# Kernel tuning notes

Measured on AMD Instinct MI355X. Metric: run time of the kernel, lower is better.

Reference implementation:

```python
import jax, jax.numpy as jnp
import numpy as np
from jax import lax

B, N, S, K = 16, 8192, 1024, 32
FACTOR = 1.0
EPS_BN = 1e-5


def farthest_point_sample(xyz, npoint):
    # xyz: [B, N, 3] -> idx [B, npoint]. Deterministic start at index 0
    # (torch version starts at a random index; start choice doesn't change the math pattern).
    b, n, _ = xyz.shape
    bidx = jnp.arange(b)

    def step(carry, _):
        distance, farthest = carry
        centroid = xyz[bidx, farthest]                      # [B, 3]
        dist = jnp.sum((xyz - centroid[:, None, :]) ** 2, -1)  # [B, N]
        distance = jnp.minimum(distance, dist)
        new_far = jnp.argmax(distance, axis=-1)
        return (distance, new_far), farthest

    init = (jnp.full((b, n), 1e10, xyz.dtype), jnp.zeros((b,), jnp.int32))
    _, idxs = lax.scan(step, init, None, length=npoint)
    return idxs.T  # [B, npoint]


def square_distance(src, dst):
    # [B,Ns,3] x [B,Nd,3] -> [B,Ns,Nd]
    d = -2.0 * jnp.einsum('bnc,bmc->bnm', src, dst)
    d += jnp.sum(src ** 2, -1)[:, :, None]
    d += jnp.sum(dst ** 2, -1)[:, None, :]
    return d


def safe_cdist(x):
    # x: [B, C, S]; pairwise euclidean over rows -> [B, C, C]; zero-safe sqrt
    diff = x[:, :, None, :] - x[:, None, :, :]          # [B, C, C, S]
    sq = jnp.sum(diff * diff, -1)
    pos = sq > 0
    return jnp.where(pos, jnp.sqrt(jnp.where(pos, sq, 1.0)), 0.0)


def batchnorm(x, gamma, beta, axes):
    mean = jnp.mean(x, axes, keepdims=True)
    var = jnp.var(x, axes, keepdims=True)  # biased, as in torch BN normalization
    return (x - mean) / jnp.sqrt(var + EPS_BN) * gamma + beta


def reference(xyz, bn1_gamma, bn1_beta, bn2_gamma, bn2_beta):
    b = xyz.shape[0]
    # --- FPS sampling ---
    fps_idx = farthest_point_sample(lax.stop_gradient(xyz), S)          # [B,S]
    new_xyz = jnp.take_along_axis(xyz, fps_idx[:, :, None], axis=1)     # [B,S,3]
    # --- kNN grouping ---
    sq = square_distance(lax.stop_gradient(new_xyz), lax.stop_gradient(xyz))  # [B,S,N]
    _, knn_idx = lax.top_k(-sq, K)                                      # [B,S,K] indices
    grouped = jax.vmap(lambda p, i: p[i])(xyz, knn_idx)                 # [B,S,K,3]
    diff = grouped - new_xyz[:, :, None, :]
    std = jnp.std(diff, ddof=1)                                         # scalar, unbiased like torch.std
    knn_norm = diff / (std + 1e-5)
    center = jnp.broadcast_to(new_xyz[:, :, None, :], (b, S, K, 3))
    knn_xyz = jnp.concatenate([knn_norm, center], axis=-1)              # [B,S,K,6]
    # --- Pooling over neighbors ---
    x = jnp.transpose(knn_xyz, (0, 3, 1, 2))                            # [B,6,S,K]
    lc = jnp.max(x, -1) + jnp.mean(x, -1)                               # [B,6,S]
    lc = jax.nn.relu(batchnorm(lc, bn1_gamma[None, :, None], bn1_beta[None, :, None], (0, 2)))
    # --- Consecutive representation (cdist + superdiagonal factor) ---
    tfcw = safe_cdist(lc)                                               # [B,6,6]
    i = jnp.arange(5)
    tfcw = tfcw.at[:, i, i + 1].multiply(FACTOR)
    # --- Pooling2 ---
    feat = tfcw.reshape(b, -1)                                          # [B,36]
    feat = jax.nn.relu(batchnorm(feat, bn2_gamma[None, :], bn2_beta[None, :], (0,)))
    return feat


def setup_inputs() -> dict:
    key = jax.random.key(0)
    k1, = jax.random.split(key, 1)
    return {
        'xyz': jax.random.normal(k1, (B, N, 3), dtype=jnp.float32),
        'bn1_gamma': jnp.ones((6,), jnp.float32),
        'bn1_beta': jnp.zeros((6,), jnp.float32),
        'bn2_gamma': jnp.ones((36,), jnp.float32),
        'bn2_beta': jnp.zeros((36,), jnp.float32),
    }
```

## Files before the change

kernel.cpp:

```cpp
#include <hip/hip_runtime.h>
#include <hip/hip_bf16.h>

constexpr int BB = 16;
constexpr int NN = 8192;
constexpr int SS = 1024;
constexpr int KK = 32;
constexpr int BUFC = 256;

__device__ __forceinline__ float b2f(__hip_bfloat16 h) { return __bfloat162float(h); }

__device__ __forceinline__ unsigned mkey32(float d) {
    unsigned u = __float_as_uint(d);
    return u ^ (0x80000000u | (unsigned)((int)u >> 31));
}

template <int CTRL, int RMASK>
__device__ __forceinline__ unsigned long long dppmove_u64(unsigned long long v) {
    int lo = (int)(unsigned)v, hi = (int)(unsigned)(v >> 32);
    int nlo = __builtin_amdgcn_update_dpp(lo, lo, CTRL, RMASK, 0xf, false);
    int nhi = __builtin_amdgcn_update_dpp(hi, hi, CTRL, RMASK, 0xf, false);
    return ((unsigned long long)(unsigned)nhi << 32) | (unsigned)nlo;
}

__device__ __forceinline__ unsigned long long u64max(unsigned long long a,
                                                     unsigned long long b) {
    return a > b ? a : b;
}

__device__ __forceinline__ unsigned long long wave_max_dpp(unsigned long long k) {
    k = u64max(k, dppmove_u64<0x121, 0xf>(k));
    k = u64max(k, dppmove_u64<0x122, 0xf>(k));
    k = u64max(k, dppmove_u64<0x124, 0xf>(k));
    k = u64max(k, dppmove_u64<0x128, 0xf>(k));
    k = u64max(k, dppmove_u64<0x142, 0xa>(k));
    k = u64max(k, dppmove_u64<0x143, 0xc>(k));
    return k;
}

__device__ __forceinline__ unsigned long long bitonic64(unsigned long long v, int lane) {
#pragma unroll
    for (int k = 2; k <= 64; k <<= 1) {
#pragma unroll
        for (int j = k >> 1; j > 0; j >>= 1) {
            unsigned long long p = __shfl_xor(v, j);
            bool up = ((lane & k) == 0);
            bool lower = ((lane & j) == 0);
            bool take_min = (up == lower);
            v = take_min ? (p < v ? p : v) : (p > v ? p : v);
        }
    }
    return v;
}

__global__ __launch_bounds__(256) void convert_kernel(
    const void* __restrict__ xyz_raw, const void* __restrict__ g1r,
    const void* __restrict__ b1r, const void* __restrict__ g2r,
    const void* __restrict__ b2r, float* __restrict__ xyzf,
    float* __restrict__ params, void* __restrict__ out_raw) {
    const unsigned short* u = (const unsigned short*)xyz_raw;
    unsigned short s = u[2 * (threadIdx.x & 63)];
    int e = (s >> 7) & 0xFF;
    unsigned long long m = __ballot(e >= 100 && e <= 140);
    bool isbf = __popcll(m) > 48;

    const int NT = BB * NN * 3;
    int tid = blockIdx.x * blockDim.x + threadIdx.x;
    int stride = gridDim.x * blockDim.x;
    if (isbf) {
        const __hip_bfloat16* p = (const __hip_bfloat16*)xyz_raw;
        for (int i = tid; i < NT; i += stride) xyzf[i] = b2f(p[i]);
    } else {
        const float* p = (const float*)xyz_raw;
        for (int i = tid; i < NT; i += stride) xyzf[i] = p[i];
    }
    if (blockIdx.x == 0 && threadIdx.x < 85) {
        int t = threadIdx.x;
        if (t == 84) {
            params[84] = isbf ? 1.0f : 0.0f;
        } else {
            const void* src; int off;
            if (t < 6)       { src = g1r; off = t; }
            else if (t < 12) { src = b1r; off = t - 6; }
            else if (t < 48) { src = g2r; off = t - 12; }
            else             { src = b2r; off = t - 48; }
            params[t] = isbf ? b2f(((const __hip_bfloat16*)src)[off])
                             : ((const float*)src)[off];
        }
    }
    if (blockIdx.x == 1 && threadIdx.x < 64) {
        for (int i = threadIdx.x; i < 576; i += 64) {
            if (isbf) ((__hip_bfloat16*)out_raw)[i] = __float2bfloat16(1.0f);
            else      ((float*)out_raw)[i] = 1.0f;
        }
    }
}

__global__ __attribute__((amdgpu_flat_work_group_size(512, 512)))
__attribute__((amdgpu_waves_per_eu(2, 2)))
void fps_kernel(const float* __restrict__ xyzf, float* __restrict__ new_xyz) {
    constexpr int T = 512, P = NN / T;
    const int b = blockIdx.x, t = threadIdx.x;
    const float* xb = xyzf + (size_t)b * NN * 3;

    __shared__ float sxyz[NN * 3];
    __shared__ unsigned long long skey[2][8];

    float px[P], py[P], pz[P], ds[P];
#pragma unroll
    for (int j = 0; j < P; j++) {
        int p = t + j * T;
        px[j] = xb[p * 3 + 0];
        py[j] = xb[p * 3 + 1];
        pz[j] = xb[p * 3 + 2];
        ds[j] = 1e10f;
    }
    for (int i = t; i < NN * 3; i += T) sxyz[i] = xb[i];

    float cx = xb[0], cy = xb[1], cz = xb[2];
    if (t == 0) {
        float* o = new_xyz + (size_t)b * SS * 3;
        o[0] = cx; o[1] = cy; o[2] = cz;
    }
    const int wave = t >> 6, lane = t & 63;
    __syncthreads();

    for (int step = 1; step < SS; step++) {
        float bv = -1.0f; int bj = 0;
#pragma unroll
        for (int j = 0; j < P; j++) {
            float dx = __fsub_rn(px[j], cx);
            float dy = __fsub_rn(py[j], cy);
            float dz = __fsub_rn(pz[j], cz);
            float d = __fadd_rn(__fadd_rn(__fmul_rn(dx, dx), __fmul_rn(dy, dy)), __fmul_rn(dz, dz));
            float mm = fminf(ds[j], d);
            ds[j] = mm;
            if (mm > bv) { bv = mm; bj = j; }
        }
        unsigned idx = (unsigned)(t + bj * T);
        unsigned long long key =
            ((unsigned long long)__float_as_uint(bv) << 32) | (unsigned)(~idx);

        key = wave_max_dpp(key);
        const int par = step & 1;
        if (lane == 63) skey[par][wave] = key;
        __syncthreads();

        unsigned long long k0 = u64max(skey[par][0], skey[par][1]);
        unsigned long long k1 = u64max(skey[par][2], skey[par][3]);
        unsigned long long k2 = u64max(skey[par][4], skey[par][5]);
        unsigned long long k3 = u64max(skey[par][6], skey[par][7]);
        unsigned long long bk = u64max(u64max(k0, k1), u64max(k2, k3));

        unsigned gidx = ~(unsigned)bk;
        cx = sxyz[gidx * 3 + 0];
        cy = sxyz[gidx * 3 + 1];
        cz = sxyz[gidx * 3 + 2];
        if (t == 0) {
            float* o = new_xyz + ((size_t)b * SS + step) * 3;
            o[0] = cx; o[1] = cy; o[2] = cz;
        }
    }
}

__global__ __launch_bounds__(256, 2) void knn_kernel(const float* __restrict__ xyzf,
                                                     const float* __restrict__ new_xyz,
                                                     float* __restrict__ A,
                                                     double* __restrict__ qstats) {
    __shared__ unsigned long long buf[4][BUFC];
    const int t = threadIdx.x;
    const int lane = t & 63, wv = t >> 6;
    const int w = blockIdx.x * 4 + wv;
    const int b = w >> 10, s = w & 1023;

    const float* q = new_xyz + ((size_t)b * SS + s) * 3;
    float qx = q[0], qy = q[1], qz = q[2];
    float qq = __fadd_rn(__fadd_rn(__fmul_rn(qx, qx), __fmul_rn(qy, qy)), __fmul_rn(qz, qz));

    const float* pb = xyzf + (size_t)b * NN * 3;

    unsigned mk[128];
    unsigned long long lmin = ~0ull;
#pragma unroll
    for (int j = 0; j < 128; j++) {
        int idx = j * 64 + lane;
        float px = pb[idx * 3 + 0];
        float py = pb[idx * 3 + 1];
        float pz = pb[idx * 3 + 2];
        float dot = __fadd_rn(__fadd_rn(__fmul_rn(qx, px), __fmul_rn(qy, py)), __fmul_rn(qz, pz));
        float pp  = __fadd_rn(__fadd_rn(__fmul_rn(px, px), __fmul_rn(py, py)), __fmul_rn(pz, pz));
        float d = __fadd_rn(__fadd_rn(__fmul_rn(-2.0f, dot), qq), pp);
        mk[j] = mkey32(d);
        unsigned long long key = ((unsigned long long)mk[j] << 32) | (unsigned)idx;
        lmin = key < lmin ? key : lmin;
    }

    unsigned long long vs = bitonic64(lmin, lane);
    unsigned long long That = __shfl(vs, 31);

    for (int i = lane; i < BUFC; i += 64) buf[wv][i] = ~0ull;
    const unsigned long long ltmask = (1ull << lane) - 1ull;
    int base = 0;
#pragma unroll
    for (int j = 0; j < 128; j++) {
        unsigned long long key = ((unsigned long long)mk[j] << 32) | (unsigned)(j * 64 + lane);
        bool f = key <= That;
        unsigned long long bal = __ballot(f);
        int pos = base + __popcll(bal & ltmask);
        if (f && pos < BUFC) buf[wv][pos] = key;
        base += __popcll(bal);
    }

    if (base > BUFC) {
        unsigned lo = 0, hi = (unsigned)(That >> 32);
        for (int it = 0; it < 32; it++) {
            unsigned mid = lo + ((hi - lo) >> 1);
            int c = 0;
#pragma unroll
            for (int j = 0; j < 128; j++) c += (mk[j] <= mid) ? 1 : 0;
#pragma unroll
            for (int o = 32; o > 0; o >>= 1) c += __shfl_xor(c, o);
            if (c >= 32) hi = mid; else lo = mid + 1;
        }
        That = ((unsigned long long)hi << 32) | 0xFFFFFFFFull;
        for (int i = lane; i < BUFC; i += 64) buf[wv][i] = ~0ull;
        base = 0;
#pragma unroll
        for (int j = 0; j < 128; j++) {
            unsigned long long key = ((unsigned long long)mk[j] << 32) | (unsigned)(j * 64 + lane);
            bool f = key <= That;
            unsigned long long bal = __ballot(f);
            int pos = base + __popcll(bal & ltmask);
            if (f && pos < BUFC) buf[wv][pos] = key;
            base += __popcll(bal);
        }
        if (base > BUFC) base = BUFC;
    }

    int M = base;
    unsigned long long kept = ~0ull;
    if (M <= 64) {
        unsigned long long v = (lane < M) ? buf[wv][lane] : ~0ull;
        v = bitonic64(v, lane);
        kept = v;
    } else {
        unsigned long long c0 = buf[wv][lane];
        unsigned long long c1 = buf[wv][64 + lane];
        unsigned long long c2 = buf[wv][128 + lane];
        unsigned long long c3 = buf[wv][192 + lane];
        for (int r = 0; r < KK; r++) {
            unsigned long long m01 = c0 < c1 ? c0 : c1;
            unsigned long long m23 = c2 < c3 ? c2 : c3;
            unsigned long long mm = m01 < m23 ? m01 : m23;
#pragma unroll
            for (int o = 32; o > 0; o >>= 1) {
                unsigned long long t2 = __shfl_xor(mm, o);
                mm = t2 < mm ? t2 : mm;
            }
            if (lane == r) kept = mm;
            c0 = (c0 == mm) ? ~0ull : c0;
            c1 = (c1 == mm) ? ~0ull : c1;
            c2 = (c2 == mm) ? ~0ull : c2;
            c3 = (c3 == mm) ? ~0ull : c3;
        }
    }

    bool act = (lane < KK);
    float gx = 0.0f, gy = 0.0f, gz = 0.0f;
    if (act) {
        unsigned nidx = (unsigned)kept;
        gx = pb[nidx * 3 + 0];
        gy = pb[nidx * 3 + 1];
        gz = pb[nidx * 3 + 2];
    }
    float dx = __fsub_rn(gx, qx);
    float dy = __fsub_rn(gy, qy);
    float dz = __fsub_rn(gz, qz);
    float mx = act ? dx : -3.402823466e38f;
    float my = act ? dy : -3.402823466e38f;
    float mz = act ? dz : -3.402823466e38f;
    float sx = act ? dx : 0.0f;
    float sy = act ? dy : 0.0f;
    float sz = act ? dz : 0.0f;
    double s1 = act ? ((double)dx + (double)dy + (double)dz) : 0.0;
    double s2 = act ? ((double)dx * dx + (double)dy * dy + (double)dz * dz) : 0.0;
#pragma unroll
    for (int o = 32; o > 0; o >>= 1) {
        mx = fmaxf(mx, __shfl_xor(mx, o));
        my = fmaxf(my, __shfl_xor(my, o));
        mz = fmaxf(mz, __shfl_xor(mz, o));
        sx += __shfl_xor(sx, o);
        sy += __shfl_xor(sy, o);
        sz += __shfl_xor(sz, o);
        s1 += __shfl_xor(s1, o);
        s2 += __shfl_xor(s2, o);
    }
    if (lane == 0) {
        float* a = A + ((size_t)b * SS + s) * 3;
        a[0] = __fadd_rn(mx, __fmul_rn(sx, 0.03125f));
        a[1] = __fadd_rn(my, __fmul_rn(sy, 0.03125f));
        a[2] = __fadd_rn(mz, __fmul_rn(sz, 0.03125f));
        qstats[2 * w + 0] = s1;
        qstats[2 * w + 1] = s2;
    }
}

__global__ __launch_bounds__(256) void reduce_stats_kernel(const double* __restrict__ qstats,
                                                           double* __restrict__ stats) {
    __shared__ double r1[4], r2[4];
    int t = threadIdx.x;
    double a = 0.0, bsum = 0.0;
    for (int i = t; i < BB * SS; i += 256) { a += qstats[2 * i]; bsum += qstats[2 * i + 1]; }
#pragma unroll
    for (int o = 32; o > 0; o >>= 1) { a += __shfl_xor(a, o); bsum += __shfl_xor(bsum, o); }
    int wv = t >> 6, ln = t & 63;
    if (ln == 0) { r1[wv] = a; r2[wv] = bsum; }
    __syncthreads();
    if (t == 0) {
        stats[0] = r1[0] + r1[1] + r1[2] + r1[3];
        stats[1] = r2[0] + r2[1] + r2[2] + r2[3];
    }
}

__global__ __launch_bounds__(256) void lc_kernel(const float* __restrict__ new_xyz,
                                                 const float* __restrict__ A,
                                                 const double* __restrict__ stats,
                                                 float* __restrict__ lc,
                                                 double* __restrict__ bn1acc) {
    __shared__ double red[4];
    const int b = blockIdx.x / 6, c = blockIdx.x % 6;
    const int t = threadIdx.x;
    const double n = (double)BB * SS * KK * 3;
    double sd = stats[0], sq = stats[1];
    double var = (sq - sd * sd / n) / (n - 1.0);
    float stdv = (float)sqrt(var);
    float denom = __fadd_rn(stdv, 1e-5f);

    double s1 = 0.0, s2 = 0.0;
    for (int r = 0; r < 4; r++) {
        int s = r * 256 + t;
        float v;
        if (c < 3) {
            v = A[((size_t)b * SS + s) * 3 + c] / denom;
        } else {
            float ww = new_xyz[((size_t)b * SS + s) * 3 + (c - 3)];
            v = __fadd_rn(ww, ww);
        }
        lc[((size_t)b * 6 + c) * SS + s] = v;
        s1 += (double)v;
        s2 += (double)v * (double)v;
    }
#pragma unroll
    for (int off = 32; off > 0; off >>= 1) { s1 += __shfl_down(s1, off); s2 += __shfl_down(s2, off); }
    int wv = t >> 6, ln = t & 63;
    if (ln == 0) red[wv] = s1;
    __syncthreads();
    if (t == 0) atomicAdd(&bn1acc[c * 2 + 0], red[0] + red[1] + red[2] + red[3]);
    __syncthreads();
    if (ln == 0) red[wv] = s2;
    __syncthreads();
    if (t == 0) atomicAdd(&bn1acc[c * 2 + 1], red[0] + red[1] + red[2] + red[3]);
}

__global__ __launch_bounds__(256) void cdist_kernel(const float* __restrict__ lc,
                                                    const double* __restrict__ bn1acc,
                                                    const float* __restrict__ params,
                                                    float* __restrict__ tf) {
    __shared__ float sy[6 * SS];
    const int b = blockIdx.x, t = threadIdx.x;
    float mean[6], sde[6], gg[6], bt[6];
    const double n = (double)BB * SS;
#pragma unroll
    for (int c = 0; c < 6; c++) {
        double m = bn1acc[c * 2 + 0] / n;
        double v = bn1acc[c * 2 + 1] / n - m * m;
        mean[c] = (float)m;
        sde[c] = sqrtf((float)v + 1e-5f);
        gg[c] = params[c];
        bt[c] = params[6 + c];
    }
    for (int r = 0; r < 24; r++) {
        int g = r * 256 + t;
        int c = g >> 10;
        float v = lc[(size_t)b * 6 * SS + g];
        float y = (v - mean[c]) / sde[c] * gg[c] + bt[c];
        sy[g] = fmaxf(y, 0.0f);
    }
    __syncthreads();
    if (t < 6) tf[b * 36 + t * 7] = 0.0f;

    const int w = t >> 6, lane = t & 63;
    const int PI[15] = {0,0,0,0,0,1,1,1,1,2,2,2,3,3,4};
    const int PJ[15] = {1,2,3,4,5,2,3,4,5,3,4,5,4,5,5};
    for (int r = 0; r < 4; r++) {
        int p = w + r * 4;
        if (p < 15) {
            int i = PI[p], j = PJ[p];
            float acc = 0.0f;
            for (int m2 = 0; m2 < 16; m2++) {
                int s = lane + m2 * 64;
                float d = sy[i * SS + s] - sy[j * SS + s];
                acc += d * d;
            }
#pragma unroll
            for (int off = 32; off > 0; off >>= 1) acc += __shfl_down(acc, off);
            if (lane == 0) {
                float v = acc > 0.0f ? sqrtf(acc) : 0.0f;
                const float FACTOR = 1.0f;
                tf[b * 36 + i * 6 + j] = (j == i + 1) ? v * FACTOR : v;
                tf[b * 36 + j * 6 + i] = v;
            }
        }
    }
}

__global__ __launch_bounds__(64) void bn2_kernel(const float* __restrict__ tf,
                                                 const float* __restrict__ params,
                                                 void* __restrict__ out_raw) {
    int f = threadIdx.x;
    if (f >= 36) return;
    bool isbf = params[84] != 0.0f;
    float x[16]; float sum = 0.0f;
#pragma unroll
    for (int b = 0; b < 16; b++) { x[b] = tf[b * 36 + f]; sum += x[b]; }
    float mean = sum * 0.0625f;
    float vs = 0.0f;
#pragma unroll
    for (int b = 0; b < 16; b++) { float d = x[b] - mean; vs += d * d; }
    float var = vs * 0.0625f;
    float denom = sqrtf(var + 1e-5f);
    float g = params[12 + f], bb = params[48 + f];
#pragma unroll
    for (int b = 0; b < 16; b++) {
        float y = (x[b] - mean) / denom * g + bb;
        y = fmaxf(y, 0.0f);
        if (isbf) ((__hip_bfloat16*)out_raw)[b * 36 + f] = __float2bfloat16(y);
        else      ((float*)out_raw)[b * 36 + f] = y;
    }
}

extern "C" void kernel_launch(void* const* d_in, const int* in_sizes, int n_in,
                              void* d_out, int out_size, void* d_ws, size_t ws_size,
                              hipStream_t stream) {
    const void* xyz_raw = d_in[0];
    const void* g1r = d_in[1]; const void* b1r = d_in[2];
    const void* g2r = d_in[3]; const void* b2r = d_in[4];
    {
        const void* six[2] = {nullptr, nullptr}; int n6 = 0;
        const void* t36[2] = {nullptr, nullptr}; int n36 = 0;
        const void* big = nullptr;
        for (int i = 0; i < n_in; i++) {
            if (in_sizes[i] == BB * NN * 3) big = d_in[i];
            else if (in_sizes[i] == 6  && n6  < 2) six[n6++]  = d_in[i];
            else if (in_sizes[i] == 36 && n36 < 2) t36[n36++] = d_in[i];
        }
        if (big && n6 == 2 && n36 == 2) {
            xyz_raw = big; g1r = six[0]; b1r = six[1]; g2r = t36[0]; b2r = t36[1];
        }
    }

    char* ws = (char*)d_ws;
    float* xyzf    = (float*)(ws + 0);
    float* new_xyz = (float*)(ws + 1572864);
    float* A       = (float*)(ws + 1769472);
    float* lc      = (float*)(ws + 1966080);
    float* tf      = (float*)(ws + 2359296);
    double* stats  = (double*)(ws + 2361600);
    double* bn1acc = stats + 2;
    float* params  = (float*)(ws + 2361712);
    double* qstats = (double*)(ws + 2362112);

    hipMemsetAsync(stats, 0, 14 * sizeof(double), stream);
    hipLaunchKernelGGL(convert_kernel, dim3(512), dim3(256), 0, stream,
                       xyz_raw, g1r, b1r, g2r, b2r, xyzf, params, d_out);
    hipLaunchKernelGGL(fps_kernel,          dim3(16),   dim3(512), 0, stream, xyzf, new_xyz);
    hipLaunchKernelGGL(knn_kernel,          dim3(4096), dim3(256), 0, stream, xyzf, new_xyz, A, qstats);
    hipLaunchKernelGGL(reduce_stats_kernel, dim3(1),    dim3(256), 0, stream, qstats, stats);
    hipLaunchKernelGGL(lc_kernel,           dim3(96),   dim3(256), 0, stream, new_xyz, A, stats, lc, bn1acc);
    hipLaunchKernelGGL(cdist_kernel,        dim3(16),   dim3(256), 0, stream, lc, bn1acc, params, tf);
    hipLaunchKernelGGL(bn2_kernel,          dim3(1),    dim3(64),  0, stream, tf, params, d_out);

    (void)in_sizes; (void)n_in; (void)out_size; (void)ws_size;
}
```

Baseline: 1.260 ms.

## Fuse FPS and kNN into one persistent kernel with progress-flag handoff

Merges the sequential farthest-point-sampling kernel and the kNN kernel into a single launch. Sixteen blocks run FPS and publish each new centroid together with a per-batch progress counter, using release stores. The remaining 240 blocks loop over queries, spin-waiting with acquire loads until their centroid is published, so kNN work overlaps the long serial FPS loop. The cost is lower kNN occupancy, since each block reserves FPS-sized shared memory and 512 threads. It also depends on all blocks being resident at once, and a bounded spin guard can let a query read a centroid that has not been written yet if FPS falls behind.

```diff
diff --git a/kernel.cpp b/kernel.cpp
--- a/kernel.cpp
+++ b/kernel.cpp
@@ -6,6 +6,8 @@
 constexpr int SS = 1024;
 constexpr int KK = 32;
 constexpr int BUFC = 256;
+constexpr int NBLK = 256;
+constexpr int NWORKW = (NBLK - BB) * 8;
 
 __device__ __forceinline__ float b2f(__hip_bfloat16 h) { return __bfloat162float(h); }
 
@@ -56,7 +58,8 @@
     const void* __restrict__ xyz_raw, const void* __restrict__ g1r,
     const void* __restrict__ b1r, const void* __restrict__ g2r,
     const void* __restrict__ b2r, float* __restrict__ xyzf,
-    float* __restrict__ params, void* __restrict__ out_raw) {
+    float* __restrict__ params, void* __restrict__ out_raw,
+    unsigned* __restrict__ prog) {
     const unsigned short* u = (const unsigned short*)xyz_raw;
     unsigned short s = u[2 * (threadIdx.x & 63)];
     int e = (s >> 7) & 0xFF;
@@ -93,214 +96,241 @@
             else      ((float*)out_raw)[i] = 1.0f;
         }
     }
+    if (blockIdx.x == 2 && threadIdx.x < 256) {
+        prog[threadIdx.x] = 0u;
+    }
 }
 
 __global__ __attribute__((amdgpu_flat_work_group_size(512, 512)))
 __attribute__((amdgpu_waves_per_eu(2, 2)))
-void fps_kernel(const float* __restrict__ xyzf, float* __restrict__ new_xyz) {
-    constexpr int T = 512, P = NN / T;
-    const int b = blockIdx.x, t = threadIdx.x;
-    const float* xb = xyzf + (size_t)b * NN * 3;
-
+void fps_knn_kernel(const float* __restrict__ xyzf,
+                    float* __restrict__ new_xyz,
+                    unsigned* __restrict__ prog,
+                    float* __restrict__ A,
+                    double* __restrict__ qstats) {
     __shared__ float sxyz[NN * 3];
     __shared__ unsigned long long skey[2][8];
-
-    float px[P], py[P], pz[P], ds[P];
-#pragma unroll
-    for (int j = 0; j < P; j++) {
-        int p = t + j * T;
-        px[j] = xb[p * 3 + 0];
-        py[j] = xb[p * 3 + 1];
-        pz[j] = xb[p * 3 + 2];
-        ds[j] = 1e10f;
-    }
-    for (int i = t; i < NN * 3; i += T) sxyz[i] = xb[i];
-
-    float cx = xb[0], cy = xb[1], cz = xb[2];
-    if (t == 0) {
-        float* o = new_xyz + (size_t)b * SS * 3;
-        o[0] = cx; o[1] = cy; o[2] = cz;
-    }
+    __shared__ unsigned long long buf[8][BUFC];
+
+    const int blk = blockIdx.x, t = threadIdx.x;
     const int wave = t >> 6, lane = t & 63;
-    __syncthreads();
-
-    for (int step = 1; step < SS; step++) {
-        float bv = -1.0f; int bj = 0;
+
+    if (blk < BB) {
+        constexpr int T = 512, P = NN / T;
+        const int b = blk;
+        const float* xb = xyzf + (size_t)b * NN * 3;
+
+        float px[P], py[P], pz[P], ds[P];
 #pragma unroll
         for (int j = 0; j < P; j++) {
-            float dx = __fsub_rn(px[j], cx);
-            float dy = __fsub_rn(py[j], cy);
-            float dz = __fsub_rn(pz[j], cz);
-            float d = __fadd_rn(__fadd_rn(__fmul_rn(dx, dx), __fmul_rn(dy, dy)), __fmul_rn(dz, dz));
-            float mm = fminf(ds[j], d);
-            ds[j] = mm;
-            if (mm > bv) { bv = mm; bj = j; }
-        }
-        unsigned idx = (unsigned)(t + bj * T);
-        unsigned long long key =
-            ((unsigned long long)__float_as_uint(bv) << 32) | (unsigned)(~idx);
-
-        key = wave_max_dpp(key);
-        const int par = step & 1;
-        if (lane == 63) skey[par][wave] = key;
+            int p = t + j * T;
+            px[j] = xb[p * 3 + 0];
+            py[j] = xb[p * 3 + 1];
+            pz[j] = xb[p * 3 + 2];
+            ds[j] = 1e10f;
+        }
+        for (int i = t; i < NN * 3; i += T) sxyz[i] = xb[i];
+
+        float cx = xb[0], cy = xb[1], cz = xb[2];
+        if (t == 0) {
+            unsigned* o = (unsigned*)(new_xyz + (size_t)b * SS * 3);
+            __hip_atomic_store(&o[0], __float_as_uint(cx), __ATOMIC_RELAXED, __HIP_MEMORY_SCOPE_AGENT);
+            __hip_atomic_store(&o[1], __float_as_uint(cy), __ATOMIC_RELAXED, __HIP_MEMORY_SCOPE_AGENT);
+            __hip_atomic_store(&o[2], __float_as_uint(cz), __ATOMIC_RELAXED, __HIP_MEMORY_SCOPE_AGENT);
+            __hip_atomic_store(&prog[b * 16], 1u, __ATOMIC_RELEASE, __HIP_MEMORY_SCOPE_AGENT);
+        }
         __syncthreads();
 
-        unsigned long long k0 = u64max(skey[par][0], skey[par][1]);
-        unsigned long long k1 = u64max(skey[par][2], skey[par][3]);
-        unsigned long long k2 = u64max(skey[par][4], skey[par][5]);
-        unsigned long long k3 = u64max(skey[par][6], skey[par][7]);
-        unsigned long long bk = u64max(u64max(k0, k1), u64max(k2, k3));
-
-        unsigned gidx = ~(unsigned)bk;
-        cx = sxyz[gidx * 3 + 0];
-        cy = sxyz[gidx * 3 + 1];
-        cz = sxyz[gidx * 3 + 2];
-        if (t == 0) {
-            float* o = new_xyz + ((size_t)b * SS + step) * 3;
-            o[0] = cx; o[1] = cy; o[2] = cz;
-        }
-    }
-}
-
-__global__ __launch_bounds__(256, 2) void knn_kernel(const float* __restrict__ xyzf,
-                                                     const float* __restrict__ new_xyz,
-                                                     float* __restrict__ A,
-                                                     double* __restrict__ qstats) {
-    __shared__ unsigned long long buf[4][BUFC];
-    const int t = threadIdx.x;
-    const int lane = t & 63, wv = t >> 6;
-    const int w = blockIdx.x * 4 + wv;
-    const int b = w >> 10, s = w & 1023;
-
-    const float* q = new_xyz + ((size_t)b * SS + s) * 3;
-    float qx = q[0], qy = q[1], qz = q[2];
-    float qq = __fadd_rn(__fadd_rn(__fmul_rn(qx, qx), __fmul_rn(qy, qy)), __fmul_rn(qz, qz));
-
-    const float* pb = xyzf + (size_t)b * NN * 3;
-
-    unsigned mk[128];
-    unsigned long long lmin = ~0ull;
-#pragma unroll
-    for (int j = 0; j < 128; j++) {
-        int idx = j * 64 + lane;
-        float px = pb[idx * 3 + 0];
-        float py = pb[idx * 3 + 1];
-        float pz = pb[idx * 3 + 2];
-        float dot = __fadd_rn(__fadd_rn(__fmul_rn(qx, px), __fmul_rn(qy, py)), __fmul_rn(qz, pz));
-        float pp  = __fadd_rn(__fadd_rn(__fmul_rn(px, px), __fmul_rn(py, py)), __fmul_rn(pz, pz));
-        float d = __fadd_rn(__fadd_rn(__fmul_rn(-2.0f, dot), qq), pp);
-        mk[j] = mkey32(d);
-        unsigned long long key = ((unsigned long long)mk[j] << 32) | (unsigned)idx;
-        lmin = key < lmin ? key : lmin;
-    }
-
-    unsigned long long vs = bitonic64(lmin, lane);
-    unsigned long long That = __shfl(vs, 31);
-
-    for (int i = lane; i < BUFC; i += 64) buf[wv][i] = ~0ull;
-    const unsigned long long ltmask = (1ull << lane) - 1ull;
-    int base = 0;
-#pragma unroll
-    for (int j = 0; j < 128; j++) {
-        unsigned long long key = ((unsigned long long)mk[j] << 32) | (unsigned)(j * 64 + lane);
-        bool f = key <= That;
-        unsigned long long bal = __ballot(f);
-        int pos = base + __popcll(bal & ltmask);
-        if (f && pos < BUFC) buf[wv][pos] = key;
-        base += __popcll(bal);
-    }
-
-    if (base > BUFC) {
-        unsigned lo = 0, hi = (unsigned)(That >> 32);
-        for (int it = 0; it < 32; it++) {
-            unsigned mid = lo + ((hi - lo) >> 1);
-            int c = 0;
-#pragma unroll
-            for (int j = 0; j < 128; j++) c += (mk[j] <= mid) ? 1 : 0;
-#pragma unroll
-            for (int o = 32; o > 0; o >>= 1) c += __shfl_xor(c, o);
-            if (c >= 32) hi = mid; else lo = mid + 1;
-        }
-        That = ((unsigned long long)hi << 32) | 0xFFFFFFFFull;
-        for (int i = lane; i < BUFC; i += 64) buf[wv][i] = ~0ull;
-        base = 0;
-#pragma unroll
-        for (int j = 0; j < 128; j++) {
-            unsigned long long key = ((unsigned long long)mk[j] << 32) | (unsigned)(j * 64 + lane);
-            bool f = key <= That;
-            unsigned long long bal = __ballot(f);
-            int pos = base + __popcll(bal & ltmask);
-            if (f && pos < BUFC) buf[wv][pos] = key;
-            base += __popcll(bal);
-        }
-        if (base > BUFC) base = BUFC;
-    }
-
-    int M = base;
-    unsigned long long kept = ~0ull;
-    if (M <= 64) {
-        unsigned long long v = (lane < M) ? buf[wv][lane] : ~0ull;
-        v = bitonic64(v, lane);
-        kept = v;
+        for (int step = 1; step < SS; step++) {
+            float bv = -1.0f; int bj = 0;
+#pragma unroll
+            for (int j = 0; j < P; j++) {
+                float dx = __fsub_rn(px[j], cx);
+                float dy = __fsub_rn(py[j], cy);
+                float dz = __fsub_rn(pz[j], cz);
+                float d = __fadd_rn(__fadd_rn(__fmul_rn(dx, dx), __fmul_rn(dy, dy)), __fmul_rn(dz, dz));
+                float mm = fminf(ds[j], d);
+                ds[j] = mm;
+                if (mm > bv) { bv = mm; bj = j; }
+            }
+            unsigned idx = (unsigned)(t + bj * T);
+            unsigned long long key =
+                ((unsigned long long)__float_as_uint(bv) << 32) | (unsigned)(~idx);
+
+            key = wave_max_dpp(key);
+            const int par = step & 1;
+            if (lane == 63) skey[par][wave] = key;
+            __syncthreads();
+
+            unsigned long long k0 = u64max(skey[par][0], skey[par][1]);
+            unsigned long long k1 = u64max(skey[par][2], skey[par][3]);
+            unsigned long long k2 = u64max(skey[par][4], skey[par][5]);
+            unsigned long long k3 = u64max(skey[par][6], skey[par][7]);
+            unsigned long long bk = u64max(u64max(k0, k1), u64max(k2, k3));
+
+            unsigned gidx = ~(unsigned)bk;
+            cx = sxyz[gidx * 3 + 0];
+            cy = sxyz[gidx * 3 + 1];
+            cz = sxyz[gidx * 3 + 2];
+            if (t == 0) {
+                unsigned* o = (unsigned*)(new_xyz + ((size_t)b * SS + step) * 3);
+                __hip_atomic_store(&o[0], __float_as_uint(cx), __ATOMIC_RELAXED, __HIP_MEMORY_SCOPE_AGENT);
+                __hip_atomic_store(&o[1], __float_as_uint(cy), __ATOMIC_RELAXED, __HIP_MEMORY_SCOPE_AGENT);
+                __hip_atomic_store(&o[2], __float_as_uint(cz), __ATOMIC_RELAXED, __HIP_MEMORY_SCOPE_AGENT);
+                __hip_atomic_store(&prog[b * 16], (unsigned)(step + 1), __ATOMIC_RELEASE, __HIP_MEMORY_SCOPE_AGENT);
+            }
+        }
     } else {
-        unsigned long long c0 = buf[wv][lane];
-        unsigned long long c1 = buf[wv][64 + lane];
-        unsigned long long c2 = buf[wv][128 + lane];
-        unsigned long long c3 = buf[wv][192 + lane];
-        for (int r = 0; r < KK; r++) {
-            unsigned long long m01 = c0 < c1 ? c0 : c1;
-            unsigned long long m23 = c2 < c3 ? c2 : c3;
-            unsigned long long mm = m01 < m23 ? m01 : m23;
+        const int w2 = (blk - BB) * 8 + wave;
+        const unsigned long long ltmask = (1ull << lane) - 1ull;
+
+        for (int qid = w2; qid < BB * SS; qid += NWORKW) {
+            const int b = qid >> 10, s = qid & 1023;
+
+            if (lane == 0) {
+                int guard = 0;
+                while (__hip_atomic_load(&prog[b * 16], __ATOMIC_ACQUIRE,
+                                         __HIP_MEMORY_SCOPE_AGENT) < (unsigned)(s + 1) &&
+                       ++guard < (1 << 16)) {
+                    __builtin_amdgcn_s_sleep(1);
+                }
+            }
+            float qx = 0.0f, qy = 0.0f, qz = 0.0f;
+            if (lane == 0) {
+                const unsigned* o = (const unsigned*)(new_xyz + (size_t)qid * 3);
+                qx = __uint_as_float(__hip_atomic_load(&o[0], __ATOMIC_RELAXED, __HIP_MEMORY_SCOPE_AGENT));
+                qy = __uint_as_float(__hip_atomic_load(&o[1], __ATOMIC_RELAXED, __HIP_MEMORY_SCOPE_AGENT));
+                qz = __uint_as_float(__hip_atomic_load(&o[2], __ATOMIC_RELAXED, __HIP_MEMORY_SCOPE_AGENT));
+            }
+            qx = __shfl(qx, 0); qy = __shfl(qy, 0); qz = __shfl(qz, 0);
+            float qq = __fadd_rn(__fadd_rn(__fmul_rn(qx, qx), __fmul_rn(qy, qy)), __fmul_rn(qz, qz));
+
+            const float* pb = xyzf + (size_t)b * NN * 3;
+
+            unsigned mk[128];
+            unsigned long long lmin = ~0ull;
+#pragma unroll
+            for (int j = 0; j < 128; j++) {
+                int idx = j * 64 + lane;
+                float px = pb[idx * 3 + 0];
+                float py = pb[idx * 3 + 1];
+                float pz = pb[idx * 3 + 2];
+                float dot = __fadd_rn(__fadd_rn(__fmul_rn(qx, px), __fmul_rn(qy, py)), __fmul_rn(qz, pz));
+                float pp  = __fadd_rn(__fadd_rn(__fmul_rn(px, px), __fmul_rn(py, py)), __fmul_rn(pz, pz));
+                float d = __fadd_rn(__fadd_rn(__fmul_rn(-2.0f, dot), qq), pp);
+                mk[j] = mkey32(d);
+                unsigned long long key = ((unsigned long long)mk[j] << 32) | (unsigned)idx;
+                lmin = key < lmin ? key : lmin;
+            }
+
+            unsigned long long vs = bitonic64(lmin, lane);
+            unsigned long long That = __shfl(vs, 31);
+
+            for (int i = lane; i < BUFC; i += 64) buf[wave][i] = ~0ull;
+            int base = 0;
+#pragma unroll
+            for (int j = 0; j < 128; j++) {
+                unsigned long long key = ((unsigned long long)mk[j] << 32) | (unsigned)(j * 64 + lane);
+                bool f = key <= That;
+                unsigned long long bal = __ballot(f);
+                int pos = base + __popcll(bal & ltmask);
+                if (f && pos < BUFC) buf[wave][pos] = key;
+                base += __popcll(bal);
+            }
+
+            if (base > BUFC) {
+                unsigned lo = 0, hi = (unsigned)(That >> 32);
+                for (int it = 0; it < 32; it++) {
+                    unsigned mid = lo + ((hi - lo) >> 1);
+                    int c = 0;
+#pragma unroll
+                    for (int j = 0; j < 128; j++) c += (mk[j] <= mid) ? 1 : 0;
+#pragma unroll
+                    for (int o = 32; o > 0; o >>= 1) c += __shfl_xor(c, o);
+                    if (c >= 32) hi = mid; else lo = mid + 1;
+                }
+                That = ((unsigned long long)hi << 32) | 0xFFFFFFFFull;
+                for (int i = lane; i < BUFC; i += 64) buf[wave][i] = ~0ull;
+                base = 0;
+#pragma unroll
+                for (int j = 0; j < 128; j++) {
+                    unsigned long long key = ((unsigned long long)mk[j] << 32) | (unsigned)(j * 64 + lane);
+                    bool f = key <= That;
+                    unsigned long long bal = __ballot(f);
+                    int pos = base + __popcll(bal & ltmask);
+                    if (f && pos < BUFC) buf[wave][pos] = key;
+                    base += __popcll(bal);
+                }
+                if (base > BUFC) base = BUFC;
+            }
+
+            int M = base;
+            unsigned long long kept = ~0ull;
+            if (M <= 64) {
+                unsigned long long v = (lane < M) ? buf[wave][lane] : ~0ull;
+                v = bitonic64(v, lane);
+                kept = v;
+            } else {
+                unsigned long long c0 = buf[wave][lane];
+                unsigned long long c1 = buf[wave][64 + lane];
+                unsigned long long c2 = buf[wave][128 + lane];
+                unsigned long long c3 = buf[wave][192 + lane];
+                for (int r = 0; r < KK; r++) {
+                    unsigned long long m01 = c0 < c1 ? c0 : c1;
+                    unsigned long long m23 = c2 < c3 ? c2 : c3;
+                    unsigned long long mm = m01 < m23 ? m01 : m23;
+#pragma unroll
+                    for (int o = 32; o > 0; o >>= 1) {
+                        unsigned long long t2 = __shfl_xor(mm, o);
+                        mm = t2 < mm ? t2 : mm;
+                    }
+                    if (lane == r) kept = mm;
+                    c0 = (c0 == mm) ? ~0ull : c0;
+                    c1 = (c1 == mm) ? ~0ull : c1;
+                    c2 = (c2 == mm) ? ~0ull : c2;
+                    c3 = (c3 == mm) ? ~0ull : c3;
+                }
+            }
+
+            bool act = (lane < KK);
+            float gx = 0.0f, gy = 0.0f, gz = 0.0f;
+            if (act) {
+                unsigned nidx = (unsigned)kept;
+                gx = pb[nidx * 3 + 0];
+                gy = pb[nidx * 3 + 1];
+                gz = pb[nidx * 3 + 2];
+            }
+            float dx = __fsub_rn(gx, qx);
+            float dy = __fsub_rn(gy, qy);
+            float dz = __fsub_rn(gz, qz);
+            float mx = act ? dx : -3.402823466e38f;
+            float my = act ? dy : -3.402823466e38f;
+            float mz = act ? dz : -3.402823466e38f;
+            float sx = act ? dx : 0.0f;
+            float sy = act ? dy : 0.0f;
+            float sz = act ? dz : 0.0f;
+            double s1 = act ? ((double)dx + (double)dy + (double)dz) : 0.0;
+            double s2 = act ? ((double)dx * dx + (double)dy * dy + (double)dz * dz) : 0.0;
 #pragma unroll
             for (int o = 32; o > 0; o >>= 1) {
-                unsigned long long t2 = __shfl_xor(mm, o);
-                mm = t2 < mm ? t2 : mm;
-            }
-            if (lane == r) kept = mm;
-            c0 = (c0 == mm) ? ~0ull : c0;
-            c1 = (c1 == mm) ? ~0ull : c1;
-            c2 = (c2 == mm) ? ~0ull : c2;
-            c3 = (c3 == mm) ? ~0ull : c3;
-        }
-    }
-
-    bool act = (lane < KK);
-    float gx = 0.0f, gy = 0.0f, gz = 0.0f;
-    if (act) {
-        unsigned nidx = (unsigned)kept;
-        gx = pb[nidx * 3 + 0];
-        gy = pb[nidx * 3 + 1];
-        gz = pb[nidx * 3 + 2];
-    }
-    float dx = __fsub_rn(gx, qx);
-    float dy = __fsub_rn(gy, qy);
-    float dz = __fsub_rn(gz, qz);
-    float mx = act ? dx : -3.402823466e38f;
-    float my = act ? dy : -3.402823466e38f;
-    float mz = act ? dz : -3.402823466e38f;
-    float sx = act ? dx : 0.0f;
-    float sy = act ? dy : 0.0f;
-    float sz = act ? dz : 0.0f;
-    double s1 = act ? ((double)dx + (double)dy + (double)dz) : 0.0;
-    double s2 = act ? ((double)dx * dx + (double)dy * dy + (double)dz * dz) : 0.0;
-#pragma unroll
-    for (int o = 32; o > 0; o >>= 1) {
-        mx = fmaxf(mx, __shfl_xor(mx, o));
-        my = fmaxf(my, __shfl_xor(my, o));
-        mz = fmaxf(mz, __shfl_xor(mz, o));
-        sx += __shfl_xor(sx, o);
-        sy += __shfl_xor(sy, o);
-        sz += __shfl_xor(sz, o);
-        s1 += __shfl_xor(s1, o);
-        s2 += __shfl_xor(s2, o);
-    }
-    if (lane == 0) {
-        float* a = A + ((size_t)b * SS + s) * 3;
-        a[0] = __fadd_rn(mx, __fmul_rn(sx, 0.03125f));
-        a[1] = __fadd_rn(my, __fmul_rn(sy, 0.03125f));
-        a[2] = __fadd_rn(mz, __fmul_rn(sz, 0.03125f));
-        qstats[2 * w + 0] = s1;
-        qstats[2 * w + 1] = s2;
+                mx = fmaxf(mx, __shfl_xor(mx, o));
+                my = fmaxf(my, __shfl_xor(my, o));
+                mz = fmaxf(mz, __shfl_xor(mz, o));
+                sx += __shfl_xor(sx, o);
+                sy += __shfl_xor(sy, o);
+                sz += __shfl_xor(sz, o);
+                s1 += __shfl_xor(s1, o);
+                s2 += __shfl_xor(s2, o);
+            }
+            if (lane == 0) {
+                float* a = A + ((size_t)b * SS + s) * 3;
+                a[0] = __fadd_rn(mx, __fmul_rn(sx, 0.03125f));
+                a[1] = __fadd_rn(my, __fmul_rn(sy, 0.03125f));
+                a[2] = __fadd_rn(mz, __fmul_rn(sz, 0.03125f));
+                qstats[2 * qid + 0] = s1;
+                qstats[2 * qid + 1] = s2;
+            }
+        }
     }
 }
 
@@ -468,12 +498,13 @@
     double* bn1acc = stats + 2;
     float* params  = (float*)(ws + 2361712);
     double* qstats = (double*)(ws + 2362112);
+    unsigned* prog = (unsigned*)tf;
 
     hipMemsetAsync(stats, 0, 14 * sizeof(double), stream);
     hipLaunchKernelGGL(convert_kernel, dim3(512), dim3(256), 0, stream,
-                       xyz_raw, g1r, b1r, g2r, b2r, xyzf, params, d_out);
-    hipLaunchKernelGGL(fps_kernel,          dim3(16),   dim3(512), 0, stream, xyzf, new_xyz);
-    hipLaunchKernelGGL(knn_kernel,          dim3(4096), dim3(256), 0, stream, xyzf, new_xyz, A, qstats);
+                       xyz_raw, g1r, b1r, g2r, b2r, xyzf, params, d_out, prog);
+    hipLaunchKernelGGL(fps_knn_kernel,      dim3(NBLK), dim3(512), 0, stream,
+                       xyzf, new_xyz, prog, A, qstats);
     hipLaunchKernelGGL(reduce_stats_kernel, dim3(1),    dim3(256), 0, stream, qstats, stats);
     hipLaunchKernelGGL(lc_kernel,           dim3(96),   dim3(256), 0, stream, new_xyz, A, stats, lc, bn1acc);
     hipLaunchKernelGGL(cdist_kernel,        dim3(16),   dim3(256), 0, stream, lc, bn1acc, params, tf);
```

Result: slower. 3.285 ms (+160.7%).
